# Kernel optimization log

Measured on AMD Instinct MI355X. Metric: run time of the kernel, lower is better.

## Reference

```python
import jax, jax.numpy as jnp
import numpy as np

B, S, D, H = 32, 512, 256, 512  # batch, seq_len, input_dim, hidden_dim (512 hardcoded in source)


def setup_inputs() -> dict:
    key = jax.random.key(0)
    ks = jax.random.split(key, 24)
    sc = 1.0 / np.sqrt(H)

    def p(k, shape):
        return (jax.random.normal(k, shape, jnp.float32) * sc).astype(jnp.float32)

    return {
        "x": jax.random.normal(ks[0], (B, S, D), jnp.float32),
        # encoder forward direction (PyTorch LSTM gate order i,f,g,o)
        "Wih_f": p(ks[1], (4 * H, D)), "Whh_f": p(ks[2], (4 * H, H)), "b_f": p(ks[3], (4 * H,)),
        # encoder reverse direction
        "Wih_r": p(ks[4], (4 * H, D)), "Whh_r": p(ks[5], (4 * H, H)), "b_r": p(ks[6], (4 * H,)),
        # decoder LSTM (input never used: decoder_input is always zeros in the source)
        "Wih_d": p(ks[7], (4 * H, H)), "Whh_d": p(ks[8], (4 * H, H)), "b_d": p(ks[9], (4 * H,)),
        # reduce_h / reduce_c
        "Wr_h": p(ks[10], (H, 2 * H)), "br_h": p(ks[11], (H,)),
        "Wr_c": p(ks[12], (H, 2 * H)), "br_c": p(ks[13], (H,)),
        # pointer attention
        "W1": p(ks[14], (H, H)), "b1": p(ks[15], (H,)),
        "W2": p(ks[16], (H, H)), "b2": p(ks[17], (H,)),
        "vt": p(ks[18], (1, H)), "bvt": p(ks[19], (1,)),
    }


def _lstm_cell(h, c, z):
    i, f, g, o = jnp.split(z, 4, axis=-1)
    c_new = jax.nn.sigmoid(f) * c + jax.nn.sigmoid(i) * jnp.tanh(g)
    h_new = jax.nn.sigmoid(o) * jnp.tanh(c_new)
    return h_new, c_new


def _run_lstm(xs, Wih, Whh, b):
    """xs: [S, B, D] -> (outputs [S,B,H], h_T [B,H], c_T [B,H])"""
    Bn = xs.shape[1]
    Hn = Whh.shape[1]
    init = (jnp.zeros((Bn, Hn), xs.dtype), jnp.zeros((Bn, Hn), xs.dtype))
    x_proj = jnp.einsum('sbd,gd->sbg', xs, Wih) + b  # precompute input contribution

    def step(carry, xp):
        h, c = carry
        h, c = _lstm_cell(h, c, xp + h @ Whh.T)
        return (h, c), h

    (hT, cT), hs = jax.lax.scan(step, init, x_proj)
    return hs, hT, cT


def reference(x, Wih_f, Whh_f, b_f, Wih_r, Whh_r, b_r,
              Wih_d, Whh_d, b_d, Wr_h, br_h, Wr_c, br_c,
              W1, b1, W2, b2, vt, bvt):
    xs = jnp.swapaxes(x, 0, 1)  # [S, B, D]
    hs_f, hf, cf = _run_lstm(xs, Wih_f, Whh_f, b_f)
    hs_r, hr, cr = _run_lstm(xs[::-1], Wih_r, Whh_r, b_r)
    hs_r = hs_r[::-1]

    h_d = jnp.concatenate([hf, hr], axis=-1) @ Wr_h.T + br_h  # [B, H]
    c_d = jnp.concatenate([cf, cr], axis=-1) @ Wr_c.T + br_c

    enc_red = hs_f + hs_r  # [S, B, H]  (enc_out[...,:512] + enc_out[...,512:])
    pre1 = jnp.einsum('sbh,kh->sbk', enc_red, W1) + b1  # W1(enc) precomputed once

    seq_len = x.shape[1]

    def dec_step(carry, _):
        h, c = carry
        # decoder_input is always zeros -> Wih_d contribution is exactly 0
        h, c = _lstm_cell(h, c, h @ Whh_d.T + b_d)
        att = jnp.tanh(pre1 + (h @ W2.T + b2)[None])      # [S, B, H]
        scores = jnp.einsum('sbh,h->sb', att, vt[0]) + bvt[0]
        return (h, c), scores.T  # [B, S]

    _, logits = jax.lax.scan(dec_step, (h_d, c_d), None, length=seq_len)
    return jnp.swapaxes(logits, 0, 1)  # [B, seq_len, S]
```

## Files before the change

kernel.cpp:

```cpp
#include <hip/hip_runtime.h>
#include <hip/hip_bf16.h>
#include <cstdint>
#include <cstddef>

#define B_ 32
#define S_ 512
#define D_ 256
#define H_ 512

typedef _Float16 h2 __attribute__((ext_vector_type(2)));
typedef _Float16 h4 __attribute__((ext_vector_type(4)));
typedef _Float16 h8 __attribute__((ext_vector_type(8)));
typedef float f32x4 __attribute__((ext_vector_type(4)));
typedef unsigned u32x4 __attribute__((ext_vector_type(4)));

__device__ __forceinline__ h2 H2(unsigned u) { return __builtin_bit_cast(h2, u); }
__device__ __forceinline__ unsigned U2(h2 v) { return __builtin_bit_cast(unsigned, v); }

#if __has_builtin(__builtin_amdgcn_exp2f)
__device__ __forceinline__ float exp2_fast(float x) { return __builtin_amdgcn_exp2f(x); }
#else
__device__ __forceinline__ float exp2_fast(float x) { return exp2f(x); }
#endif
#if __has_builtin(__builtin_amdgcn_rcpf)
__device__ __forceinline__ float rcp_fast(float x) { return __builtin_amdgcn_rcpf(x); }
#else
__device__ __forceinline__ float rcp_fast(float x) { return 1.0f / x; }
#endif

__device__ __forceinline__ float sigm(float x) {
  return rcp_fast(1.0f + exp2_fast(-1.4426950408889634f * x));
}
__device__ __forceinline__ float tanh_fast(float x) {
  return 1.0f - 2.0f * rcp_fast(1.0f + exp2_fast(2.8853900817779268f * x));
}

__device__ __forceinline__ uint4 coh_load16(const void* p) {
  u32x4 v;
  asm volatile("global_load_dwordx4 %0, %1, off sc0 sc1"
               : "=v"(v) : "v"(p) : "memory");
  return __builtin_bit_cast(uint4, v);
}
__device__ __forceinline__ void vm_drain() {
  asm volatile("s_waitcnt vmcnt(0)" ::: "memory");
}

__device__ __forceinline__ bool valid16(uint4 v) {
  return ((v.x & 0xFFFFu) != 0xFFFFu) && ((v.x >> 16) != 0xFFFFu) &&
         ((v.y & 0xFFFFu) != 0xFFFFu) && ((v.y >> 16) != 0xFFFFu) &&
         ((v.z & 0xFFFFu) != 0xFFFFu) && ((v.z >> 16) != 0xFFFFu) &&
         ((v.w & 0xFFFFu) != 0xFFFFu) && ((v.w >> 16) != 0xFFFFu);
}

__device__ __forceinline__ void h_store(unsigned short* p, unsigned short v) {
  __hip_atomic_store(p, v, __ATOMIC_RELAXED, __HIP_MEMORY_SCOPE_AGENT);
}

#define N_X   1048576u
#define N_WIH 131072u
#define N_WHH 262144u
#define N_W1  65536u
#define C0_ N_X
#define C1_ (C0_ + N_WIH)
#define C2_ (C1_ + N_WIH)
#define C3_ (C2_ + N_WHH)
#define C4_ (C3_ + N_WHH)
#define C5_ (C4_ + N_WHH)
#define C6_ (C5_ + N_W1)
#define NCV (C6_ + N_W1)
__global__ __launch_bounds__(256) void prep_k(
    const float* __restrict__ x,
    const float* __restrict__ WihF, const float* __restrict__ WihR,
    const float* __restrict__ WhhF, const float* __restrict__ WhhR,
    const float* __restrict__ WhhD,
    const float* __restrict__ W1, const float* __restrict__ W2,
    _Float16* __restrict__ xh, _Float16* __restrict__ wihF, _Float16* __restrict__ wihR,
    _Float16* __restrict__ whhF, _Float16* __restrict__ whhR, _Float16* __restrict__ whhD,
    _Float16* __restrict__ w1h, _Float16* __restrict__ w2h,
    uint4* __restrict__ sent)
{
  const size_t stride = (size_t)gridDim.x * 256;
  const size_t NS = 3ull * S_ * B_ * H_ / 8;
  uint4 sv = {0xFFFFFFFFu, 0xFFFFFFFFu, 0xFFFFFFFFu, 0xFFFFFFFFu};
  for (size_t j = (size_t)blockIdx.x * 256 + threadIdx.x; j < NS; j += stride)
    sent[j] = sv;
  for (size_t j = (size_t)blockIdx.x * 256 + threadIdx.x; j < NCV; j += stride) {
    const float* src; _Float16* dst; size_t off;
    if (j < C0_)      { src = x;    dst = xh;   off = j; }
    else if (j < C1_) { src = WihF; dst = wihF; off = j - C0_; }
    else if (j < C2_) { src = WihR; dst = wihR; off = j - C1_; }
    else if (j < C3_) { src = WhhF; dst = whhF; off = j - C2_; }
    else if (j < C4_) { src = WhhR; dst = whhR; off = j - C3_; }
    else if (j < C5_) { src = WhhD; dst = whhD; off = j - C4_; }
    else if (j < C6_) { src = W1;   dst = w1h;  off = j - C5_; }
    else              { src = W2;   dst = w2h;  off = j - C6_; }
    float4 v = ((const float4*)src)[off];
    h4 o = {(_Float16)v.x, (_Float16)v.y, (_Float16)v.z, (_Float16)v.w};
    ((h4*)dst)[off] = o;
  }
}

__global__ __launch_bounds__(256, 1) void enc_coop_k(
    const _Float16* __restrict__ xh,
    const _Float16* __restrict__ WihF, const _Float16* __restrict__ WhhF, const float* __restrict__ bF,
    const _Float16* __restrict__ WihR, const _Float16* __restrict__ WhhR, const float* __restrict__ bR,
    float* __restrict__ cF, float* __restrict__ cR,
    _Float16* __restrict__ hsF, _Float16* __restrict__ hsR)
{
  __shared__ __align__(16) _Float16 cbuf[96][16][8];
  __shared__ float zfin[4][16][17];
  __shared__ float cls[16][17];

  const int bid = blockIdx.x;
  const int group = bid >> 5;
  const int dir = group >> 1;
  const int bh0 = (group & 1) << 4;
  const int jb = bid & 31;
  const int c0 = jb << 4;
  const int tid = threadIdx.x;
  const int lane = tid & 63;
  const int wv = tid >> 6;

  const _Float16* __restrict__ Wih = dir ? WihR : WihF;
  const _Float16* __restrict__ Whh = dir ? WhhR : WhhF;
  const float* __restrict__ bias = dir ? bR : bF;
  _Float16* __restrict__ hs = dir ? hsR : hsF;
  float* __restrict__ cOut = dir ? cR : cF;

  h8 aw[24];
  {
    const int m = lane & 15, kg = lane >> 4;
    const int wrow = wv * H_ + c0 + m;
    const _Float16* wi = Wih + (size_t)wrow * D_;
    const _Float16* wh = Whh + (size_t)wrow * H_;
    #pragma unroll
    for (int tu = 0; tu < 24; ++tu) {
      int k = tu * 32 + kg * 8;
      aw[tu] = (k < 256) ? *(const h8*)(wi + k) : *(const h8*)(wh + (k - 256));
    }
  }

  const int cc = tid & 15, cb = tid >> 4;
  float bvg[4];
  #pragma unroll
  for (int g = 0; g < 4; ++g) bvg[g] = bias[g * H_ + c0 + cc];

  const char* cbase = (const char*)cbuf + (size_t)((lane >> 4) * 256 + (lane & 15) * 16);
  const int sn = tid & 15;
  const int xo = (tid >> 4) * 2;
  const int ho = (tid >> 4) * 4;
  __syncthreads();

  for (int t = 0; t < S_; ++t) {
    const int xi = dir ? (S_ - 1 - t) : t;

    {
      const _Float16* xp = xh + ((size_t)(bh0 + sn) * S_ + xi) * D_;
      uint4 v0 = *(const uint4*)(xp + xo * 8);
      uint4 v1 = *(const uint4*)(xp + xo * 8 + 8);
      *(uint4*)&cbuf[xo][sn][0] = v0;
      *(uint4*)&cbuf[xo + 1][sn][0] = v1;
    }
    __syncthreads();

    f32x4 acc0 = {0.f, 0.f, 0.f, 0.f}, acc1 = {0.f, 0.f, 0.f, 0.f};
    #pragma unroll
    for (int tu = 0; tu < 8; tu += 2) {
      h8 b0 = *(const h8*)(cbase + tu * 1024);
      h8 b1 = *(const h8*)(cbase + (tu + 1) * 1024);
      acc0 = __builtin_amdgcn_mfma_f32_16x16x32_f16(aw[tu], b0, acc0, 0, 0, 0);
      acc1 = __builtin_amdgcn_mfma_f32_16x16x32_f16(aw[tu + 1], b1, acc1, 0, 0, 0);
    }

    {
      if (t == 0) {
        uint4 z = {0, 0, 0, 0};
        #pragma unroll
        for (int u = 0; u < 4; ++u) *(uint4*)&cbuf[32 + ho + u][sn][0] = z;
      } else {
        const int xip = dir ? xi + 1 : xi - 1;
        const _Float16* hbase = hs + ((size_t)xip * B_ + bh0 + sn) * H_;
        uint4 vs[4];
        unsigned pend = 0xF;
        do {
          #pragma unroll
          for (int u = 0; u < 4; ++u)
            if (pend & (1u << u)) vs[u] = coh_load16(hbase + (ho + u) * 8);
          vm_drain();
          #pragma unroll
          for (int u = 0; u < 4; ++u)
            if ((pend & (1u << u)) && valid16(vs[u])) pend &= ~(1u << u);
        } while (pend);
        #pragma unroll
        for (int u = 0; u < 4; ++u) *(uint4*)&cbuf[32 + ho + u][sn][0] = vs[u];
      }
    }
    __syncthreads();

    #pragma unroll
    for (int tu = 8; tu < 24; tu += 2) {
      h8 b0 = *(const h8*)(cbase + tu * 1024);
      h8 b1 = *(const h8*)(cbase + (tu + 1) * 1024);
      acc0 = __builtin_amdgcn_mfma_f32_16x16x32_f16(aw[tu], b0, acc0, 0, 0, 0);
      acc1 = __builtin_amdgcn_mfma_f32_16x16x32_f16(aw[tu + 1], b1, acc1, 0, 0, 0);
    }
    {
      const int mrow = (lane >> 4) * 4, n = lane & 15;
      #pragma unroll
      for (int r = 0; r < 4; ++r) zfin[wv][mrow + r][n] = acc0[r] + acc1[r];
    }
    __syncthreads();

    {
      const float zi = zfin[0][cc][cb] + bvg[0];
      const float zf = zfin[1][cc][cb] + bvg[1];
      const float zg = zfin[2][cc][cb] + bvg[2];
      const float zo = zfin[3][cc][cb] + bvg[3];
      const float c_old = (t == 0) ? 0.f : cls[cc][cb];
      const float cn = sigm(zf) * c_old + sigm(zi) * tanh_fast(zg);
      const float hn = sigm(zo) * tanh_fast(cn);
      cls[cc][cb] = cn;
      _Float16 hh = (_Float16)hn;
      h_store((unsigned short*)(hs + ((size_t)xi * B_ + bh0 + cb) * H_ + c0 + cc),
              __builtin_bit_cast(unsigned short, hh));
      if (t == S_ - 1) cOut[(size_t)(bh0 + cb) * H_ + c0 + cc] = cn;
    }
  }
}

__global__ __launch_bounds__(256, 1) void dec_coop_k(
    const float* __restrict__ hd0, const float* __restrict__ cD0,
    const _Float16* __restrict__ Whh, const float* __restrict__ bias,
    _Float16* __restrict__ hdec)
{
  __shared__ __align__(16) _Float16 cbuf[64][16][8];
  __shared__ float zfin[4][16][17];
  __shared__ float cls[16][17];

  const int bid = blockIdx.x;
  const int group = bid >> 5;
  const int bh0 = group << 4;
  const int jb = bid & 31;
  const int c0 = jb << 4;
  const int tid = threadIdx.x;
  const int lane = tid & 63;
  const int wv = tid >> 6;

  h8 aw[16];
  {
    const int m = lane & 15, kg = lane >> 4;
    const _Float16* wh = Whh + (size_t)(wv * H_ + c0 + m) * H_;
    #pragma unroll
    for (int tu = 0; tu < 16; ++tu) aw[tu] = *(const h8*)(wh + tu * 32 + kg * 8);
  }

  const int cc = tid & 15, cb = tid >> 4;
  float bvg[4];
  #pragma unroll
  for (int g = 0; g < 4; ++g) bvg[g] = bias[g * H_ + c0 + cc];
  cls[cc][cb] = cD0[(size_t)(bh0 + cb) * H_ + c0 + cc];

  const char* cbase = (const char*)cbuf + (size_t)((lane >> 4) * 256 + (lane & 15) * 16);
  const int sn = tid & 15, ho = (tid >> 4) * 4;
  __syncthreads();

  for (int t = 0; t < S_; ++t) {
    {
      if (t == 0) {
        const float* src = hd0 + (size_t)(bh0 + sn) * H_;
        #pragma unroll
        for (int u = 0; u < 4; ++u) {
          float4 f0 = *(const float4*)(src + (ho + u) * 8);
          float4 f1 = *(const float4*)(src + (ho + u) * 8 + 4);
          h8 o = {(_Float16)f0.x, (_Float16)f0.y, (_Float16)f0.z, (_Float16)f0.w,
                  (_Float16)f1.x, (_Float16)f1.y, (_Float16)f1.z, (_Float16)f1.w};
          *(h8*)&cbuf[ho + u][sn][0] = o;
        }
      } else {
        const _Float16* src = hdec + ((size_t)(t - 1) * B_ + bh0 + sn) * H_;
        uint4 vs[4];
        unsigned pend = 0xF;
        do {
          #pragma unroll
          for (int u = 0; u < 4; ++u)
            if (pend & (1u << u)) vs[u] = coh_load16(src + (ho + u) * 8);
          vm_drain();
          #pragma unroll
          for (int u = 0; u < 4; ++u)
            if ((pend & (1u << u)) && valid16(vs[u])) pend &= ~(1u << u);
        } while (pend);
        #pragma unroll
        for (int u = 0; u < 4; ++u) *(uint4*)&cbuf[ho + u][sn][0] = vs[u];
      }
    }
    __syncthreads();

    f32x4 acc0 = {0.f, 0.f, 0.f, 0.f}, acc1 = {0.f, 0.f, 0.f, 0.f};
    #pragma unroll
    for (int tu = 0; tu < 16; tu += 2) {
      h8 b0 = *(const h8*)(cbase + tu * 1024);
      h8 b1 = *(const h8*)(cbase + (tu + 1) * 1024);
      acc0 = __builtin_amdgcn_mfma_f32_16x16x32_f16(aw[tu], b0, acc0, 0, 0, 0);
      acc1 = __builtin_amdgcn_mfma_f32_16x16x32_f16(aw[tu + 1], b1, acc1, 0, 0, 0);
    }
    {
      const int mrow = (lane >> 4) * 4, n = lane & 15;
      #pragma unroll
      for (int r = 0; r < 4; ++r) zfin[wv][mrow + r][n] = acc0[r] + acc1[r];
    }
    __syncthreads();

    {
      const float zi = zfin[0][cc][cb] + bvg[0];
      const float zf = zfin[1][cc][cb] + bvg[1];
      const float zg = zfin[2][cc][cb] + bvg[2];
      const float zo = zfin[3][cc][cb] + bvg[3];
      const float cn = sigm(zf) * cls[cc][cb] + sigm(zi) * tanh_fast(zg);
      const float hn = sigm(zo) * tanh_fast(cn);
      cls[cc][cb] = cn;
      _Float16 hh = (_Float16)hn;
      h_store((unsigned short*)(hdec + ((size_t)t * B_ + bh0 + cb) * H_ + c0 + cc),
              __builtin_bit_cast(unsigned short, hh));
    }
  }
}

template <int MODE>
__global__ __launch_bounds__(256) void gemm_mfma_k(
    const _Float16* __restrict__ A1, const _Float16* __restrict__ A2,
    const _Float16* __restrict__ W, const float* __restrict__ bias,
    _Float16* __restrict__ C)
{
  __shared__ __align__(16) _Float16 Abuf[4][66][8];
  __shared__ __align__(16) _Float16 Bbuf[4][66][8];
  const int tid = threadIdx.x;
  const int m0 = blockIdx.x * 64, n0 = blockIdx.y * 64;
  const int lane = tid & 63, wv = tid >> 6;
  const int sr = tid >> 2, sk = tid & 3;
  f32x4 acc[4] = {{0.f,0.f,0.f,0.f},{0.f,0.f,0.f,0.f},
                  {0.f,0.f,0.f,0.f},{0.f,0.f,0.f,0.f}};

  for (int kc = 0; kc < H_; kc += 32) {
    __syncthreads();
    {
      uint4 a = *(const uint4*)(A1 + (size_t)(m0 + sr) * H_ + kc + sk * 8);
      if (MODE == 1) {
        uint4 a2 = *(const uint4*)(A2 + (size_t)(m0 + sr) * H_ + kc + sk * 8);
        a.x = U2(H2(a.x) + H2(a2.x)); a.y = U2(H2(a.y) + H2(a2.y));
        a.z = U2(H2(a.z) + H2(a2.z)); a.w = U2(H2(a.w) + H2(a2.w));
      }
      *(uint4*)&Abuf[sk][sr][0] = a;
      uint4 b = *(const uint4*)(W + (size_t)(n0 + sr) * H_ + kc + sk * 8);
      *(uint4*)&Bbuf[sk][sr][0] = b;
    }
    __syncthreads();
    const int fr = lane & 15, kg = lane >> 4;
    h8 af = *(const h8*)&Abuf[kg][wv * 16 + fr][0];
    #pragma unroll
    for (int nt = 0; nt < 4; ++nt) {
      h8 bf = *(const h8*)&Bbuf[kg][nt * 16 + fr][0];
      acc[nt] = __builtin_amdgcn_mfma_f32_16x16x32_f16(af, bf, acc[nt], 0, 0, 0);
    }
  }
  const int fr = lane & 15, fq = lane >> 4;
  #pragma unroll
  for (int nt = 0; nt < 4; ++nt) {
    const int n = n0 + nt * 16 + fr;
    const float bv = bias[n];
    #pragma unroll
    for (int r = 0; r < 4; ++r) {
      const int m = m0 + wv * 16 + fq * 4 + r;
      C[(size_t)m * H_ + n] = (_Float16)(acc[nt][r] + bv);
    }
  }
}

__device__ __forceinline__ float4 load4f(const float* p) { return *(const float4*)p; }
__device__ __forceinline__ float4 load4f(const _Float16* p) {
  uint2 u = *(const uint2*)p;
  h2 a = H2(u.x), b = H2(u.y);
  return make_float4((float)a.x, (float)a.y, (float)b.x, (float)b.y);
}

__global__ __launch_bounds__(256) void dec_init_k(
    const _Float16* __restrict__ hfl, const _Float16* __restrict__ hr,
    const float* __restrict__ cF, const float* __restrict__ cR,
    const float* __restrict__ Wr_h, const float* __restrict__ br_h,
    const float* __restrict__ Wr_c, const float* __restrict__ br_c,
    float* __restrict__ hd0, float* __restrict__ cD)
{
  const int tid = threadIdx.x;
  const int col = tid & 31;
  const int rg  = tid >> 5;
  const int which = (int)blockIdx.y >> 4;
  const int n = ((int)blockIdx.y & 15) * 32 + col;
  const float* W = which ? Wr_c : Wr_h;
  const float* bias = which ? br_c : br_h;
  float* C = which ? cD : hd0;
  float acc[4] = {0, 0, 0, 0};
  #pragma unroll
  for (int pass = 0; pass < 2; ++pass) {
    const float4* __restrict__ w4 = (const float4*)(W + (size_t)n * 1024 + pass * 512);
    if (which) {
      const float* A = pass ? cR : cF;
      for (int k4 = 0; k4 < 128; ++k4) {
        float4 w = w4[k4];
        #pragma unroll
        for (int i = 0; i < 4; ++i) {
          int row = rg + (i << 3);
          float4 a = load4f(A + (size_t)row * H_ + k4 * 4);
          acc[i] += w.x * a.x + w.y * a.y + w.z * a.z + w.w * a.w;
        }
      }
    } else {
      const _Float16* A = pass ? hr : hfl;
      for (int k4 = 0; k4 < 128; ++k4) {
        float4 w = w4[k4];
        #pragma unroll
        for (int i = 0; i < 4; ++i) {
          int row = rg + (i << 3);
          float4 a = load4f(A + (size_t)row * H_ + k4 * 4);
          acc[i] += w.x * a.x + w.y * a.y + w.z * a.z + w.w * a.w;
        }
      }
    }
  }
  const float bv = bias[n];
  #pragma unroll
  for (int i = 0; i < 4; ++i) {
    int row = rg + (i << 3);
    C[(size_t)row * H_ + n] = acc[i] + bv;
  }
}

__global__ __launch_bounds__(256) void sumv_k(const float* __restrict__ vt,
                                              float* __restrict__ o) {
  __shared__ float sh[4];
  float v = vt[threadIdx.x] + vt[threadIdx.x + 256];
  #pragma unroll
  for (int d = 32; d; d >>= 1) v += __shfl_down(v, d, 64);
  if ((threadIdx.x & 63) == 0) sh[threadIdx.x >> 6] = v;
  __syncthreads();
  if (threadIdx.x == 0) o[0] = sh[0] + sh[1] + sh[2] + sh[3];
}

#define KT_ 2.8853900817779268f
__global__ __launch_bounds__(256) void attn_k(
    const _Float16* __restrict__ pre1, const _Float16* __restrict__ Qm,
    const float* __restrict__ vt, const float* __restrict__ bvt,
    const float* __restrict__ sumv, float* __restrict__ out)
{
  __shared__ float sp[16][260];
  __shared__ float sq[16][260];
  __shared__ float sv[256];
  const int b = blockIdx.z, tbase = blockIdx.y << 4, sbase = blockIdx.x << 4;
  const int tid = threadIdx.x;
  const int so = tid & 15, to = tid >> 4;
  float acc0 = 0.f, acc1 = 0.f;
  const float cfin = sumv[0] + bvt[0];

  for (int h0 = 0; h0 < H_; h0 += 256) {
    __syncthreads();
    {
      const int i = tid & 15, hoo = (tid >> 4) * 16;
      const _Float16* qp = Qm + ((size_t)(tbase + i) * B_ + b) * H_ + h0 + hoo;
      const _Float16* pp = pre1 + ((size_t)(sbase + i) * B_ + b) * H_ + h0 + hoo;
      h8 q0 = *(const h8*)qp, q1 = *(const h8*)(qp + 8);
      h8 p0 = *(const h8*)pp, p1 = *(const h8*)(pp + 8);
      #pragma unroll
      for (int j = 0; j < 8; ++j) {
        sq[i][hoo + j]     = exp2_fast(fminf(fmaxf(KT_ * (float)q0[j], -60.f), 60.f));
        sq[i][hoo + 8 + j] = exp2_fast(fminf(fmaxf(KT_ * (float)q1[j], -60.f), 60.f));
        sp[i][hoo + j]     = exp2_fast(fminf(fmaxf(KT_ * (float)p0[j], -60.f), 60.f));
        sp[i][hoo + 8 + j] = exp2_fast(fminf(fmaxf(KT_ * (float)p1[j], -60.f), 60.f));
      }
    }
    sv[tid] = vt[h0 + tid];
    __syncthreads();
    #pragma unroll 8
    for (int h4_ = 0; h4_ < 64; ++h4_) {
      float4 p = *(const float4*)&sp[so][h4_ * 4];
      float4 q = *(const float4*)&sq[to][h4_ * 4];
      float4 vv = *(const float4*)&sv[h4_ * 4];
      acc0 = fmaf(vv.x, rcp_fast(fmaf(p.x, q.x, 1.0f)), acc0);
      acc1 = fmaf(vv.y, rcp_fast(fmaf(p.y, q.y, 1.0f)), acc1);
      acc0 = fmaf(vv.z, rcp_fast(fmaf(p.z, q.z, 1.0f)), acc0);
      acc1 = fmaf(vv.w, rcp_fast(fmaf(p.w, q.w, 1.0f)), acc1);
    }
  }
  out[((size_t)b * S_ + tbase + to) * S_ + sbase + so] = cfin - 2.f * (acc0 + acc1);
}

extern "C" void kernel_launch(void* const* d_in, const int* in_sizes, int n_in,
                              void* d_out, int out_size, void* d_ws, size_t ws_size,
                              hipStream_t stream)
{
  (void)in_sizes; (void)n_in; (void)out_size; (void)ws_size;
  const float* x     = (const float*)d_in[0];
  const float* WihF  = (const float*)d_in[1];
  const float* WhhF  = (const float*)d_in[2];
  const float* bF    = (const float*)d_in[3];
  const float* WihR  = (const float*)d_in[4];
  const float* WhhR  = (const float*)d_in[5];
  const float* bR    = (const float*)d_in[6];
  const float* WhhD  = (const float*)d_in[8];
  const float* bD    = (const float*)d_in[9];
  const float* Wr_h  = (const float*)d_in[10];
  const float* br_h  = (const float*)d_in[11];
  const float* Wr_c  = (const float*)d_in[12];
  const float* br_c  = (const float*)d_in[13];
  const float* W1    = (const float*)d_in[14];
  const float* b1    = (const float*)d_in[15];
  const float* W2    = (const float*)d_in[16];
  const float* b2    = (const float*)d_in[17];
  const float* vt    = (const float*)d_in[18];
  const float* bvt   = (const float*)d_in[19];
  float* out = (float*)d_out;

  const size_t SBH = (size_t)S_ * B_ * H_;
  const size_t BH  = (size_t)B_ * H_;

  _Float16* hp = (_Float16*)d_ws;
  _Float16* hs_f  = hp;              hp += SBH;
  _Float16* hs_r  = hp;              hp += SBH;
  _Float16* hdec  = hp;              hp += SBH;
  _Float16* pre1h = hp;              hp += SBH;
  _Float16* Qmh   = hp;              hp += SBH;
  _Float16* xh    = hp;              hp += (size_t)B_ * S_ * D_;
  _Float16* wihF  = hp;              hp += (size_t)4 * H_ * D_;
  _Float16* wihR  = hp;              hp += (size_t)4 * H_ * D_;
  _Float16* whhF  = hp;              hp += (size_t)4 * H_ * H_;
  _Float16* whhR  = hp;              hp += (size_t)4 * H_ * H_;
  _Float16* whhD  = hp;              hp += (size_t)4 * H_ * H_;
  _Float16* w1h   = hp;              hp += (size_t)H_ * H_;
  _Float16* w2h   = hp;              hp += (size_t)H_ * H_;
  float* fp  = (float*)hp;
  float* cF  = fp;                   fp += BH;
  float* cR  = fp;                   fp += BH;
  float* cD  = fp;                   fp += BH;
  float* hd0 = fp;                   fp += BH;
  float* sumv = fp;

  prep_k<<<2048, 256, 0, stream>>>(x, WihF, WihR, WhhF, WhhR, WhhD, W1, W2,
                                   xh, wihF, wihR, whhF, whhR, whhD, w1h, w2h,
                                   (uint4*)hs_f);
  sumv_k<<<1, 256, 0, stream>>>(vt, sumv);

  enc_coop_k<<<128, 256, 0, stream>>>(xh, wihF, whhF, bF, wihR, whhR, bR,
                                      cF, cR, hs_f, hs_r);

  dec_init_k<<<dim3(1, 32), 256, 0, stream>>>(
      hs_f + (size_t)(S_ - 1) * BH, hs_r, cF, cR,
      Wr_h, br_h, Wr_c, br_c, hd0, cD);

  gemm_mfma_k<1><<<dim3(256, 8), 256, 0, stream>>>(hs_f, hs_r, w1h, b1, pre1h);

  dec_coop_k<<<64, 256, 0, stream>>>(hd0, cD, whhD, bD, hdec);

  gemm_mfma_k<0><<<dim3(256, 8), 256, 0, stream>>>(hdec, nullptr, w2h, b2, Qmh);

  attn_k<<<dim3(32, 32, 32), 256, 0, stream>>>(pre1h, Qmh, vt, bvt, sumv, out);
}
```

Before: 3.331 ms.

## Overlap pre1 GEMM with decoder recurrence in a single fused launch

Merges the W1 projection GEMM (enc_red @ W1) into the decoder cooperative kernel as extra blocks beyond the first 64, so the GEMM runs on otherwise idle CUs while the 64-block sequential decoder recurrence proceeds. This hides the GEMM latency behind the latency-bound decoder loop and removes one kernel launch. The risk is that the GEMM blocks compete for CUs or memory bandwidth with the decoder blocks, or delay their scheduling. The decoder blocks rely on co-residency (cross-block sync) and have the lowest block indices, so they should be dispatched first. The larger shared memory footprint per block may reduce occupancy for the GEMM part.

```diff
diff --git a/kernel.cpp b/kernel.cpp
--- a/kernel.cpp
+++ b/kernel.cpp
@@ -228,23 +228,69 @@
   }
 }
 
-__global__ __launch_bounds__(256, 1) void dec_coop_k(
+__global__ __launch_bounds__(256, 1) void dec_fused_k(
     const float* __restrict__ hd0, const float* __restrict__ cD0,
     const _Float16* __restrict__ Whh, const float* __restrict__ bias,
-    _Float16* __restrict__ hdec)
+    _Float16* __restrict__ hdec,
+    const _Float16* __restrict__ A1, const _Float16* __restrict__ A2,
+    const _Float16* __restrict__ W1, const float* __restrict__ b1,
+    _Float16* __restrict__ pre1)
 {
   __shared__ __align__(16) _Float16 cbuf[64][16][8];
   __shared__ float zfin[4][16][17];
   __shared__ float cls[16][17];
+  __shared__ __align__(16) _Float16 Abuf[4][66][8];
+  __shared__ __align__(16) _Float16 Bbuf[4][66][8];
+
+  const int tid = threadIdx.x;
+  const int lane = tid & 63;
+  const int wv = tid >> 6;
+
+  if (blockIdx.x >= 64) {
+    const int gb = blockIdx.x - 64;
+    const int m0 = (gb >> 3) * 64, n0 = (gb & 7) * 64;
+    const int sr = tid >> 2, sk = tid & 3;
+    f32x4 acc[4] = {{0.f,0.f,0.f,0.f},{0.f,0.f,0.f,0.f},
+                    {0.f,0.f,0.f,0.f},{0.f,0.f,0.f,0.f}};
+    for (int kc = 0; kc < H_; kc += 32) {
+      __syncthreads();
+      {
+        uint4 a = *(const uint4*)(A1 + (size_t)(m0 + sr) * H_ + kc + sk * 8);
+        uint4 a2 = *(const uint4*)(A2 + (size_t)(m0 + sr) * H_ + kc + sk * 8);
+        a.x = U2(H2(a.x) + H2(a2.x)); a.y = U2(H2(a.y) + H2(a2.y));
+        a.z = U2(H2(a.z) + H2(a2.z)); a.w = U2(H2(a.w) + H2(a2.w));
+        *(uint4*)&Abuf[sk][sr][0] = a;
+        uint4 b = *(const uint4*)(W1 + (size_t)(n0 + sr) * H_ + kc + sk * 8);
+        *(uint4*)&Bbuf[sk][sr][0] = b;
+      }
+      __syncthreads();
+      const int fr = lane & 15, kg = lane >> 4;
+      h8 af = *(const h8*)&Abuf[kg][wv * 16 + fr][0];
+      #pragma unroll
+      for (int nt = 0; nt < 4; ++nt) {
+        h8 bf = *(const h8*)&Bbuf[kg][nt * 16 + fr][0];
+        acc[nt] = __builtin_amdgcn_mfma_f32_16x16x32_f16(af, bf, acc[nt], 0, 0, 0);
+      }
+    }
+    const int fr = lane & 15, fq = lane >> 4;
+    #pragma unroll
+    for (int nt = 0; nt < 4; ++nt) {
+      const int n = n0 + nt * 16 + fr;
+      const float bv = b1[n];
+      #pragma unroll
+      for (int r = 0; r < 4; ++r) {
+        const int m = m0 + wv * 16 + fq * 4 + r;
+        pre1[(size_t)m * H_ + n] = (_Float16)(acc[nt][r] + bv);
+      }
+    }
+    return;
+  }
 
   const int bid = blockIdx.x;
   const int group = bid >> 5;
   const int bh0 = group << 4;
   const int jb = bid & 31;
   const int c0 = jb << 4;
-  const int tid = threadIdx.x;
-  const int lane = tid & 63;
-  const int wv = tid >> 6;
 
   h8 aw[16];
   {
@@ -325,9 +371,8 @@
   }
 }
 
-template <int MODE>
 __global__ __launch_bounds__(256) void gemm_mfma_k(
-    const _Float16* __restrict__ A1, const _Float16* __restrict__ A2,
+    const _Float16* __restrict__ A1,
     const _Float16* __restrict__ W, const float* __restrict__ bias,
     _Float16* __restrict__ C)
 {
@@ -344,11 +389,6 @@
     __syncthreads();
     {
       uint4 a = *(const uint4*)(A1 + (size_t)(m0 + sr) * H_ + kc + sk * 8);
-      if (MODE == 1) {
-        uint4 a2 = *(const uint4*)(A2 + (size_t)(m0 + sr) * H_ + kc + sk * 8);
-        a.x = U2(H2(a.x) + H2(a2.x)); a.y = U2(H2(a.y) + H2(a2.y));
-        a.z = U2(H2(a.z) + H2(a2.z)); a.w = U2(H2(a.w) + H2(a2.w));
-      }
       *(uint4*)&Abuf[sk][sr][0] = a;
       uint4 b = *(const uint4*)(W + (size_t)(n0 + sr) * H_ + kc + sk * 8);
       *(uint4*)&Bbuf[sk][sr][0] = b;
@@ -553,11 +593,10 @@
       hs_f + (size_t)(S_ - 1) * BH, hs_r, cF, cR,
       Wr_h, br_h, Wr_c, br_c, hd0, cD);
 
-  gemm_mfma_k<1><<<dim3(256, 8), 256, 0, stream>>>(hs_f, hs_r, w1h, b1, pre1h);
-
-  dec_coop_k<<<64, 256, 0, stream>>>(hd0, cD, whhD, bD, hdec);
-
-  gemm_mfma_k<0><<<dim3(256, 8), 256, 0, stream>>>(hdec, nullptr, w2h, b2, Qmh);
+  dec_fused_k<<<64 + 2048, 256, 0, stream>>>(hd0, cD, whhD, bD, hdec,
+                                             hs_f, hs_r, w1h, b1, pre1h);
+
+  gemm_mfma_k<<<dim3(256, 8), 256, 0, stream>>>(hdec, w2h, b2, Qmh);
 
   attn_k<<<dim3(32, 32, 32), 256, 0, stream>>>(pre1h, Qmh, vt, bvt, sumv, out);
 }
```

Result: no change. 3.290 ms (-1.2%).
